# Kernel optimization log

Hardware: AMD Instinct MI355X
Metric: run time of the kernel (lower is better)

Reference implementation:

```python
import jax, jax.numpy as jnp
import numpy as np

B, L, D = 128, 256, 1024


def setup_inputs() -> dict:
    key = jax.random.key(0)
    k = jax.random.split(key, 6)
    return {
        "tok0": jax.random.normal(k[0], (B, L, D), jnp.float32),
        "tok1": jax.random.normal(k[1], (B, L, D), jnp.float32),
        "glob0": jax.random.normal(k[2], (B, D), jnp.float32),
        "glob1": jax.random.normal(k[3], (B, D), jnp.float32),
        "len0": jax.random.randint(k[4], (B,), 0, L),
        "len1": jax.random.randint(k[5], (B,), 0, L),
    }


def _side_sums(tok, glob, lens):
    """JSD expectations for one view.

    Equivalent to the original ragged concat + dense mask construction:
    non-positive entries of get_positive_expectation contribute
    -softplus(0) + log2 = 0, and positive entries of
    get_negative_expectation contribute softplus(0) + 0 - log2 = 0,
    so only the masked terms below survive. Padding tokens (l >= lens[b])
    never exist in the original concatenated matrix, so they are excluded.
    """
    b, l_max = tok.shape[0], tok.shape[1]
    # scores: token x sentence-global, [B, L, B]
    res = jnp.einsum("bld,gd->blg", tok, glob)
    valid = jnp.arange(l_max)[None, :] < lens[:, None]          # [B, L]
    same = jnp.eye(b, dtype=bool)[:, None, :]                    # [B, 1, B]
    pos = valid[:, :, None] & same                               # token vs own sentence
    neg = valid[:, :, None] & ~same                              # token vs other sentences
    e_pos = jnp.sum(jnp.where(pos, -jax.nn.softplus(-res), 0.0))
    e_neg = jnp.sum(jnp.where(neg, jax.nn.softplus(-res) + res, 0.0))
    return e_pos, e_neg


def reference(tok0, tok1, glob0, glob1, len0, len1):
    len0 = jnp.clip(len0, 1, None)
    len1 = jnp.clip(len1, 1, None)
    avg_sentence_length = (jnp.mean(len0.astype(jnp.float32))
                           + jnp.mean(len1.astype(jnp.float32))) / 2.0

    ep0, en0 = _side_sums(tok0, glob0, len0)
    ep1, en1 = _side_sums(tok1, glob1, len1)

    num_nodes = (jnp.sum(len0) + jnp.sum(len1)).astype(jnp.float32)
    num_graphs = jnp.float32(B)
    e_pos = (ep0 + ep1) / num_nodes
    e_neg = (en0 + en1) / (num_nodes * (num_graphs - 1.0))
    loss = e_neg - e_pos
    return loss, avg_sentence_length
```

## Files before the change

kernel.cpp:

```cpp
#include <hip/hip_runtime.h>
#include <hip/hip_bf16.h>

#define B_SENT 128
#define L_TOK  256
#define D_DIM  1024
#define TM     64
#define BK     32
#define NKB    (D_DIM / BK)

typedef __attribute__((ext_vector_type(8))) short bf16x8;
typedef __attribute__((ext_vector_type(4))) float f32x4;

__device__ __forceinline__ unsigned short f2bf(float f) {
    return __builtin_bit_cast(unsigned short, __float2bfloat16(f));
}
__device__ __forceinline__ float softplus_f(float x) {
    float ax = fabsf(x);
    return fmaxf(x, 0.0f) + __logf(1.0f + __expf(-ax));
}
__device__ __forceinline__ bf16x8 cvt8f(const float4& lo, const float4& hi) {
    bf16x8 u;
    u[0] = (short)f2bf(lo.x); u[1] = (short)f2bf(lo.y);
    u[2] = (short)f2bf(lo.z); u[3] = (short)f2bf(lo.w);
    u[4] = (short)f2bf(hi.x); u[5] = (short)f2bf(hi.y);
    u[6] = (short)f2bf(hi.z); u[7] = (short)f2bf(hi.w);
    return u;
}

__device__ __forceinline__ void gl_lds16(const void* g, void* l) {
    __builtin_amdgcn_global_load_lds(
        (const __attribute__((address_space(1))) unsigned int*)g,
        (__attribute__((address_space(3))) unsigned int*)l, 16, 0, 0);
}

__global__ __launch_bounds__(256) void pack_g_kernel(
    const float* __restrict__ g0, const float* __restrict__ g1,
    short* __restrict__ packed)
{
    const int idx  = blockIdx.x * 256 + threadIdx.x;
    const int lane = idx & 63;
    const int n    = (idx >> 6) & 7;
    const int kb   = (idx >> 9) & 31;
    const int side = idx >> 14;
    const int row  = n * 16 + (lane & 15);
    const int col  = kb * 32 + (lane >> 4) * 8;
    const float* g = side ? g1 : g0;
    const float4 v0 = *reinterpret_cast<const float4*>(&g[(size_t)row * D_DIM + col]);
    const float4 v1 = *reinterpret_cast<const float4*>(&g[(size_t)row * D_DIM + col + 4]);
    *reinterpret_cast<bf16x8*>(&packed[(size_t)idx * 8]) = cvt8f(v0, v1);
}

__global__ __launch_bounds__(256, 4) void mi_main_kernel(
    const float* __restrict__ tok0, const float* __restrict__ tok1,
    const int* __restrict__ len0, const int* __restrict__ len1,
    const short* __restrict__ packed, float* __restrict__ acc_ws)
{
    const int side = blockIdx.y;
    const float* tok = side ? tok1 : tok0;
    const int*   len = side ? len1 : len0;

    const int tile   = blockIdx.x;
    const int tb     = tile * TM;
    const int b_sent = tile >> 2;
    const int count  = max(1, len[b_sent]) - (tile & 3) * TM;
    if (count <= 0) return;

    const int tid  = threadIdx.x;
    const int wave = tid >> 6;
    const int lane = tid & 63;
    const int lrow = lane & 15;
    const int kgrp = lane >> 4;

    __shared__ float As[2][2048];
    __shared__ short Bs[2][4096];
    __shared__ float sred[8];

    const float* asrc = tok + (size_t)(tb + wave * 16 + lrow) * D_DIM + kgrp * 8;
    const short* bchunk = packed + (size_t)side * NKB * 4096;
    const int br0 = ((wave * 2 + 0) * 64 + lane) * 8;
    const int br1 = ((wave * 2 + 1) * 64 + lane) * 8;

    f32x4 acc[8];
#pragma unroll
    for (int n = 0; n < 8; ++n) acc[n] = (f32x4){0.f, 0.f, 0.f, 0.f};

    auto stage = [&](int buf, int kb) {
        const float* a = asrc + kb * BK;
        gl_lds16(a,     &As[buf][(wave * 2 + 0) * 256]);
        gl_lds16(a + 4, &As[buf][(wave * 2 + 1) * 256]);
        const short* bc = bchunk + (size_t)kb * 4096;
        gl_lds16(bc + br0, &Bs[buf][(wave * 2 + 0) * 512]);
        gl_lds16(bc + br1, &Bs[buf][(wave * 2 + 1) * 512]);
    };

    auto compute = [&](int buf) {
        const f32x4 alo = *reinterpret_cast<const f32x4*>(
            &As[buf][(wave * 2 + 0) * 256 + lane * 4]);
        const f32x4 ahi = *reinterpret_cast<const f32x4*>(
            &As[buf][(wave * 2 + 1) * 256 + lane * 4]);
        bf16x8 af;
        af[0] = (short)f2bf(alo[0]); af[1] = (short)f2bf(alo[1]);
        af[2] = (short)f2bf(alo[2]); af[3] = (short)f2bf(alo[3]);
        af[4] = (short)f2bf(ahi[0]); af[5] = (short)f2bf(ahi[1]);
        af[6] = (short)f2bf(ahi[2]); af[7] = (short)f2bf(ahi[3]);
#pragma unroll
        for (int n = 0; n < 8; ++n) {
            bf16x8 b = *reinterpret_cast<const bf16x8*>(&Bs[buf][(n * 64 + lane) * 8]);
            acc[n] = __builtin_amdgcn_mfma_f32_16x16x32_bf16(af, b, acc[n], 0, 0, 0);
        }
    };

    stage(0, 0);
    __syncthreads();
#pragma unroll 1
    for (int kb = 0; kb < NKB; ++kb) {
        const int cur = kb & 1;
        if (kb + 1 < NKB) stage(cur ^ 1, kb + 1);
        compute(cur);
        __syncthreads();
    }

    float ep = 0.f, en = 0.f;
#pragma unroll
    for (int n = 0; n < 8; ++n) {
        const int g = n * 16 + lrow;
#pragma unroll
        for (int j = 0; j < 4; ++j) {
            const int rl = wave * 16 + kgrp * 4 + j;
            if (rl < count) {
                float res = acc[n][j];
                float sp  = softplus_f(res);
                if (g == b_sent) ep += res - sp;
                else             en += sp;
            }
        }
    }

#pragma unroll
    for (int off = 32; off; off >>= 1) {
        ep += __shfl_down(ep, off);
        en += __shfl_down(en, off);
    }
    if (lane == 0) { sred[wave * 2] = ep; sred[wave * 2 + 1] = en; }
    __syncthreads();
    if (tid == 0) {
        float tep = sred[0] + sred[2] + sred[4] + sred[6];
        float ten = sred[1] + sred[3] + sred[5] + sred[7];
        atomicAdd(&acc_ws[side * 2 + 0], tep);
        atomicAdd(&acc_ws[side * 2 + 1], ten);
    }
}

__global__ void mi_finalize_kernel(const int* __restrict__ len0,
                                   const int* __restrict__ len1,
                                   const float* __restrict__ acc_ws,
                                   float* __restrict__ out)
{
    const int lane = threadIdx.x;
    int s0 = 0, s1 = 0;
    for (int i = lane; i < B_SENT; i += 64) {
        s0 += max(1, len0[i]);
        s1 += max(1, len1[i]);
    }
#pragma unroll
    for (int off = 32; off; off >>= 1) {
        s0 += __shfl_down(s0, off);
        s1 += __shfl_down(s1, off);
    }
    if (lane == 0) {
        const float num_nodes = (float)(s0 + s1);
        const float ep = acc_ws[0] + acc_ws[2];
        const float en = acc_ws[1] + acc_ws[3];
        out[0] = en / (num_nodes * (float)(B_SENT - 1)) - ep / num_nodes;
        out[1] = ((float)s0 + (float)s1) / (2.0f * (float)B_SENT);
    }
}

extern "C" void kernel_launch(void* const* d_in, const int* in_sizes, int n_in,
                              void* d_out, int out_size, void* d_ws, size_t ws_size,
                              hipStream_t stream) {
    const float* tok0  = (const float*)d_in[0];
    const float* tok1  = (const float*)d_in[1];
    const float* glob0 = (const float*)d_in[2];
    const float* glob1 = (const float*)d_in[3];
    const int*   len0  = (const int*)d_in[4];
    const int*   len1  = (const int*)d_in[5];
    float* out = (float*)d_out;

    float* acc    = (float*)d_ws;
    short* packed = (short*)((char*)d_ws + 256);

    hipMemsetAsync(d_ws, 0, 256, stream);
    pack_g_kernel<<<128, 256, 0, stream>>>(glob0, glob1, packed);

    dim3 grid(32768 / TM, 2);
    mi_main_kernel<<<grid, 256, 0, stream>>>(tok0, tok1, len0, len1, packed, acc);
    mi_finalize_kernel<<<1, 64, 0, stream>>>(len0, len1, acc, out);
}
```

Baseline: 62.76 us.

## Use 128-row tiles with 512 threads and triple-buffered LDS pipeline

Doubles the token tile to 128 rows per block with 8 waves, so each packed glob chunk loaded into LDS is shared by twice as many rows. The double buffer with full __syncthreads becomes a three-stage ring using explicit vmcnt waits and a raw barrier, which lets two stages of loads stay in flight while computing. Rows past the sentence length are clamped to the last valid row so no out-of-range memory is read. Larger blocks coarsen the skipping of padded tiles, so more wasted MFMA work is done on ragged lengths, and the larger LDS footprint may reduce occupancy.

```diff
diff --git a/kernel.cpp b/kernel.cpp
--- a/kernel.cpp
+++ b/kernel.cpp
@@ -4,12 +4,14 @@
 #define B_SENT 128
 #define L_TOK  256
 #define D_DIM  1024
-#define TM     64
+#define TM     128
 #define BK     32
 #define NKB    (D_DIM / BK)
 
 typedef __attribute__((ext_vector_type(8))) short bf16x8;
 typedef __attribute__((ext_vector_type(4))) float f32x4;
+
+#define WAITVM(N) asm volatile("s_waitcnt vmcnt(" #N ")" ::: "memory")
 
 __device__ __forceinline__ unsigned short f2bf(float f) {
     return __builtin_bit_cast(unsigned short, __float2bfloat16(f));
@@ -50,7 +52,7 @@
     *reinterpret_cast<bf16x8*>(&packed[(size_t)idx * 8]) = cvt8f(v0, v1);
 }
 
-__global__ __launch_bounds__(256, 4) void mi_main_kernel(
+__global__ __launch_bounds__(512, 4) void mi_main_kernel(
     const float* __restrict__ tok0, const float* __restrict__ tok1,
     const int* __restrict__ len0, const int* __restrict__ len1,
     const short* __restrict__ packed, float* __restrict__ acc_ws)
@@ -60,9 +62,10 @@
     const int*   len = side ? len1 : len0;
 
     const int tile   = blockIdx.x;
-    const int tb     = tile * TM;
-    const int b_sent = tile >> 2;
-    const int count  = max(1, len[b_sent]) - (tile & 3) * TM;
+    const int b_sent = tile >> 1;
+    const int half   = tile & 1;
+    const int tb     = b_sent * L_TOK + half * TM;
+    const int count  = max(1, len[b_sent]) - half * TM;
     if (count <= 0) return;
 
     const int tid  = threadIdx.x;
@@ -71,14 +74,14 @@
     const int lrow = lane & 15;
     const int kgrp = lane >> 4;
 
-    __shared__ float As[2][2048];
-    __shared__ short Bs[2][4096];
-    __shared__ float sred[8];
-
-    const float* asrc = tok + (size_t)(tb + wave * 16 + lrow) * D_DIM + kgrp * 8;
+    __shared__ float As[3][4096];
+    __shared__ short Bs[3][4096];
+    __shared__ float sred[16];
+
+    const int arow = min(wave * 16 + lrow, count - 1);
+    const float* asrc = tok + (size_t)(tb + arow) * D_DIM + kgrp * 8;
     const short* bchunk = packed + (size_t)side * NKB * 4096;
-    const int br0 = ((wave * 2 + 0) * 64 + lane) * 8;
-    const int br1 = ((wave * 2 + 1) * 64 + lane) * 8;
+    const int boff = (wave * 64 + lane) * 8;
 
     f32x4 acc[8];
 #pragma unroll
@@ -88,9 +91,7 @@
         const float* a = asrc + kb * BK;
         gl_lds16(a,     &As[buf][(wave * 2 + 0) * 256]);
         gl_lds16(a + 4, &As[buf][(wave * 2 + 1) * 256]);
-        const short* bc = bchunk + (size_t)kb * 4096;
-        gl_lds16(bc + br0, &Bs[buf][(wave * 2 + 0) * 512]);
-        gl_lds16(bc + br1, &Bs[buf][(wave * 2 + 1) * 512]);
+        gl_lds16(bchunk + (size_t)kb * 4096 + boff, &Bs[buf][wave * 512]);
     };
 
     auto compute = [&](int buf) {
@@ -111,14 +112,19 @@
     };
 
     stage(0, 0);
-    __syncthreads();
+    stage(1, 1);
 #pragma unroll 1
-    for (int kb = 0; kb < NKB; ++kb) {
-        const int cur = kb & 1;
-        if (kb + 1 < NKB) stage(cur ^ 1, kb + 1);
-        compute(cur);
-        __syncthreads();
-    }
+    for (int kb = 0; kb < NKB - 1; ++kb) {
+        WAITVM(3);
+        __builtin_amdgcn_s_barrier();
+        asm volatile("" ::: "memory");
+        if (kb + 2 < NKB) stage((kb + 2) % 3, kb + 2);
+        compute(kb % 3);
+    }
+    WAITVM(0);
+    __builtin_amdgcn_s_barrier();
+    asm volatile("" ::: "memory");
+    compute((NKB - 1) % 3);
 
     float ep = 0.f, en = 0.f;
 #pragma unroll
@@ -144,8 +150,9 @@
     if (lane == 0) { sred[wave * 2] = ep; sred[wave * 2 + 1] = en; }
     __syncthreads();
     if (tid == 0) {
-        float tep = sred[0] + sred[2] + sred[4] + sred[6];
-        float ten = sred[1] + sred[3] + sred[5] + sred[7];
+        float tep = 0.f, ten = 0.f;
+#pragma unroll
+        for (int w = 0; w < 8; ++w) { tep += sred[w * 2]; ten += sred[w * 2 + 1]; }
         atomicAdd(&acc_ws[side * 2 + 0], tep);
         atomicAdd(&acc_ws[side * 2 + 1], ten);
     }
@@ -194,6 +201,6 @@
     pack_g_kernel<<<128, 256, 0, stream>>>(glob0, glob1, packed);
 
     dim3 grid(32768 / TM, 2);
-    mi_main_kernel<<<grid, 256, 0, stream>>>(tok0, tok1, len0, len1, packed, acc);
+    mi_main_kernel<<<grid, 512, 0, stream>>>(tok0, tok1, len0, len1, packed, acc);
     mi_finalize_kernel<<<1, 64, 0, stream>>>(len0, len1, acc, out);
 }
```

New measurement: 56.28 us. 10.3% less time.

## Split N across two blocks, deepen LDS pipeline to four stages, clamp padded rows

Applied to the files above, without the earlier changes.

Each token tile is now handled by two blocks, each covering half of the 128 sentence columns. This doubles the grid and halves per-block MFMA work and accumulators, but each A tile is loaded twice. The K loop moves from a double buffer with __syncthreads to a 4-deep buffer that keeps three global-to-LDS loads in flight, using explicit vmcnt waits and barriers. Rows past the sentence length are clamped to a valid row, which avoids reading tokens that will be masked anyway.

```diff
diff --git a/kernel.cpp b/kernel.cpp
--- a/kernel.cpp
+++ b/kernel.cpp
@@ -5,8 +5,10 @@
 #define L_TOK  256
 #define D_DIM  1024
 #define TM     64
+#define TN     64
 #define BK     32
 #define NKB    (D_DIM / BK)
+#define NBUF   4
 
 typedef __attribute__((ext_vector_type(8))) short bf16x8;
 typedef __attribute__((ext_vector_type(4))) float f32x4;
@@ -18,12 +20,12 @@
     float ax = fabsf(x);
     return fmaxf(x, 0.0f) + __logf(1.0f + __expf(-ax));
 }
-__device__ __forceinline__ bf16x8 cvt8f(const float4& lo, const float4& hi) {
+__device__ __forceinline__ bf16x8 cvt8f(const f32x4& lo, const f32x4& hi) {
     bf16x8 u;
-    u[0] = (short)f2bf(lo.x); u[1] = (short)f2bf(lo.y);
-    u[2] = (short)f2bf(lo.z); u[3] = (short)f2bf(lo.w);
-    u[4] = (short)f2bf(hi.x); u[5] = (short)f2bf(hi.y);
-    u[6] = (short)f2bf(hi.z); u[7] = (short)f2bf(hi.w);
+    u[0] = (short)f2bf(lo[0]); u[1] = (short)f2bf(lo[1]);
+    u[2] = (short)f2bf(lo[2]); u[3] = (short)f2bf(lo[3]);
+    u[4] = (short)f2bf(hi[0]); u[5] = (short)f2bf(hi[1]);
+    u[6] = (short)f2bf(hi[2]); u[7] = (short)f2bf(hi[3]);
     return u;
 }
 
@@ -45,8 +47,8 @@
     const int row  = n * 16 + (lane & 15);
     const int col  = kb * 32 + (lane >> 4) * 8;
     const float* g = side ? g1 : g0;
-    const float4 v0 = *reinterpret_cast<const float4*>(&g[(size_t)row * D_DIM + col]);
-    const float4 v1 = *reinterpret_cast<const float4*>(&g[(size_t)row * D_DIM + col + 4]);
+    const f32x4 v0 = *reinterpret_cast<const f32x4*>(&g[(size_t)row * D_DIM + col]);
+    const f32x4 v1 = *reinterpret_cast<const f32x4*>(&g[(size_t)row * D_DIM + col + 4]);
     *reinterpret_cast<bf16x8*>(&packed[(size_t)idx * 8]) = cvt8f(v0, v1);
 }
 
@@ -59,9 +61,11 @@
     const float* tok = side ? tok1 : tok0;
     const int*   len = side ? len1 : len0;
 
-    const int tile   = blockIdx.x;
-    const int tb     = tile * TM;
+    const int bx     = blockIdx.x;
+    const int tile   = bx >> 1;
+    const int nh     = bx & 1;
     const int b_sent = tile >> 2;
+    const int tb     = b_sent * L_TOK + (tile & 3) * TM;
     const int count  = max(1, len[b_sent]) - (tile & 3) * TM;
     if (count <= 0) return;
 
@@ -71,26 +75,24 @@
     const int lrow = lane & 15;
     const int kgrp = lane >> 4;
 
-    __shared__ float As[2][2048];
-    __shared__ short Bs[2][4096];
+    __shared__ float As[NBUF][2048];
+    __shared__ short Bs[NBUF][2048];
     __shared__ float sred[8];
 
-    const float* asrc = tok + (size_t)(tb + wave * 16 + lrow) * D_DIM + kgrp * 8;
+    const int arow = min(wave * 16 + lrow, count - 1);
+    const float* asrc = tok + (size_t)(tb + arow) * D_DIM + kgrp * 8;
     const short* bchunk = packed + (size_t)side * NKB * 4096;
-    const int br0 = ((wave * 2 + 0) * 64 + lane) * 8;
-    const int br1 = ((wave * 2 + 1) * 64 + lane) * 8;
-
-    f32x4 acc[8];
-#pragma unroll
-    for (int n = 0; n < 8; ++n) acc[n] = (f32x4){0.f, 0.f, 0.f, 0.f};
+    const int boff = ((nh * 4 + wave) * 64 + lane) * 8;
+
+    f32x4 acc[4];
+#pragma unroll
+    for (int n = 0; n < 4; ++n) acc[n] = (f32x4){0.f, 0.f, 0.f, 0.f};
 
     auto stage = [&](int buf, int kb) {
         const float* a = asrc + kb * BK;
         gl_lds16(a,     &As[buf][(wave * 2 + 0) * 256]);
         gl_lds16(a + 4, &As[buf][(wave * 2 + 1) * 256]);
-        const short* bc = bchunk + (size_t)kb * 4096;
-        gl_lds16(bc + br0, &Bs[buf][(wave * 2 + 0) * 512]);
-        gl_lds16(bc + br1, &Bs[buf][(wave * 2 + 1) * 512]);
+        gl_lds16(bchunk + (size_t)kb * 4096 + boff, &Bs[buf][wave * 512]);
     };
 
     auto compute = [&](int buf) {
@@ -98,32 +100,38 @@
             &As[buf][(wave * 2 + 0) * 256 + lane * 4]);
         const f32x4 ahi = *reinterpret_cast<const f32x4*>(
             &As[buf][(wave * 2 + 1) * 256 + lane * 4]);
-        bf16x8 af;
-        af[0] = (short)f2bf(alo[0]); af[1] = (short)f2bf(alo[1]);
-        af[2] = (short)f2bf(alo[2]); af[3] = (short)f2bf(alo[3]);
-        af[4] = (short)f2bf(ahi[0]); af[5] = (short)f2bf(ahi[1]);
-        af[6] = (short)f2bf(ahi[2]); af[7] = (short)f2bf(ahi[3]);
-#pragma unroll
-        for (int n = 0; n < 8; ++n) {
+        const bf16x8 af = cvt8f(alo, ahi);
+#pragma unroll
+        for (int n = 0; n < 4; ++n) {
             bf16x8 b = *reinterpret_cast<const bf16x8*>(&Bs[buf][(n * 64 + lane) * 8]);
             acc[n] = __builtin_amdgcn_mfma_f32_16x16x32_bf16(af, b, acc[n], 0, 0, 0);
         }
     };
 
+#define WAITSTEP(N) do {                                                     \
+        asm volatile("s_waitcnt vmcnt(" #N ")" ::: "memory");                \
+        __builtin_amdgcn_s_barrier();                                        \
+        __builtin_amdgcn_sched_barrier(0);                                   \
+    } while (0)
+
     stage(0, 0);
-    __syncthreads();
+    stage(1, 1);
+    stage(2, 2);
 #pragma unroll 1
-    for (int kb = 0; kb < NKB; ++kb) {
-        const int cur = kb & 1;
-        if (kb + 1 < NKB) stage(cur ^ 1, kb + 1);
-        compute(cur);
-        __syncthreads();
-    }
+    for (int kb = 0; kb < NKB - 3; ++kb) {
+        WAITSTEP(6);
+        stage((kb + 3) & 3, kb + 3);
+        compute(kb & 3);
+    }
+    WAITSTEP(6); compute((NKB - 3) & 3);
+    WAITSTEP(3); compute((NKB - 2) & 3);
+    WAITSTEP(0); compute((NKB - 1) & 3);
+#undef WAITSTEP
 
     float ep = 0.f, en = 0.f;
 #pragma unroll
-    for (int n = 0; n < 8; ++n) {
-        const int g = n * 16 + lrow;
+    for (int n = 0; n < 4; ++n) {
+        const int g = nh * TN + n * 16 + lrow;
 #pragma unroll
         for (int j = 0; j < 4; ++j) {
             const int rl = wave * 16 + kgrp * 4 + j;
@@ -193,7 +201,7 @@
     hipMemsetAsync(d_ws, 0, 256, stream);
     pack_g_kernel<<<128, 256, 0, stream>>>(glob0, glob1, packed);
 
-    dim3 grid(32768 / TM, 2);
+    dim3 grid(1024, 2);
     mi_main_kernel<<<grid, 256, 0, stream>>>(tok0, tok1, len0, len1, packed, acc);
     mi_finalize_kernel<<<1, 64, 0, stream>>>(len0, len1, acc, out);
 }
```

Result: slower. 102.8 us (+63.8%).

## Split K across eight waves with 16-row tiles and an LDS tree reduction

Applied to the files above, without the earlier changes.

The main kernel now works on 16-token tiles with 512 threads. Each of the eight waves handles a 128-wide slice of the D dimension, loading its A and B fragments straight from global memory into registers instead of staging them through double-buffered LDS. The partial accumulators are then combined with a three-level LDS tree reduction before the softplus epilogue. Finer tiles skip more padding rows and the K-split exposes more parallelism, but each block re-reads all of packed B, which raises L2 traffic, and the kernel holds many live registers.

```diff
diff --git a/kernel.cpp b/kernel.cpp
--- a/kernel.cpp
+++ b/kernel.cpp
@@ -4,9 +4,7 @@
 #define B_SENT 128
 #define L_TOK  256
 #define D_DIM  1024
-#define TM     64
-#define BK     32
-#define NKB    (D_DIM / BK)
+#define TM     16
 
 typedef __attribute__((ext_vector_type(8))) short bf16x8;
 typedef __attribute__((ext_vector_type(4))) float f32x4;
@@ -18,19 +16,13 @@
     float ax = fabsf(x);
     return fmaxf(x, 0.0f) + __logf(1.0f + __expf(-ax));
 }
-__device__ __forceinline__ bf16x8 cvt8f(const float4& lo, const float4& hi) {
+__device__ __forceinline__ bf16x8 cvt8f(const f32x4& lo, const f32x4& hi) {
     bf16x8 u;
-    u[0] = (short)f2bf(lo.x); u[1] = (short)f2bf(lo.y);
-    u[2] = (short)f2bf(lo.z); u[3] = (short)f2bf(lo.w);
-    u[4] = (short)f2bf(hi.x); u[5] = (short)f2bf(hi.y);
-    u[6] = (short)f2bf(hi.z); u[7] = (short)f2bf(hi.w);
+    u[0] = (short)f2bf(lo[0]); u[1] = (short)f2bf(lo[1]);
+    u[2] = (short)f2bf(lo[2]); u[3] = (short)f2bf(lo[3]);
+    u[4] = (short)f2bf(hi[0]); u[5] = (short)f2bf(hi[1]);
+    u[6] = (short)f2bf(hi[2]); u[7] = (short)f2bf(hi[3]);
     return u;
-}
-
-__device__ __forceinline__ void gl_lds16(const void* g, void* l) {
-    __builtin_amdgcn_global_load_lds(
-        (const __attribute__((address_space(1))) unsigned int*)g,
-        (__attribute__((address_space(3))) unsigned int*)l, 16, 0, 0);
 }
 
 __global__ __launch_bounds__(256) void pack_g_kernel(
@@ -45,12 +37,12 @@
     const int row  = n * 16 + (lane & 15);
     const int col  = kb * 32 + (lane >> 4) * 8;
     const float* g = side ? g1 : g0;
-    const float4 v0 = *reinterpret_cast<const float4*>(&g[(size_t)row * D_DIM + col]);
-    const float4 v1 = *reinterpret_cast<const float4*>(&g[(size_t)row * D_DIM + col + 4]);
+    const f32x4 v0 = *reinterpret_cast<const f32x4*>(&g[(size_t)row * D_DIM + col]);
+    const f32x4 v1 = *reinterpret_cast<const f32x4*>(&g[(size_t)row * D_DIM + col + 4]);
     *reinterpret_cast<bf16x8*>(&packed[(size_t)idx * 8]) = cvt8f(v0, v1);
 }
 
-__global__ __launch_bounds__(256, 4) void mi_main_kernel(
+__global__ __launch_bounds__(512, 2) void mi_main_kernel(
     const float* __restrict__ tok0, const float* __restrict__ tok1,
     const int* __restrict__ len0, const int* __restrict__ len1,
     const short* __restrict__ packed, float* __restrict__ acc_ws)
@@ -60,10 +52,11 @@
     const int*   len = side ? len1 : len0;
 
     const int tile   = blockIdx.x;
-    const int tb     = tile * TM;
-    const int b_sent = tile >> 2;
-    const int count  = max(1, len[b_sent]) - (tile & 3) * TM;
+    const int b_sent = tile >> 4;
+    const int toff   = (tile & 15) * TM;
+    const int count  = max(1, len[b_sent]) - toff;
     if (count <= 0) return;
+    const int tb     = b_sent * L_TOK + toff;
 
     const int tid  = threadIdx.x;
     const int wave = tid >> 6;
@@ -71,83 +64,94 @@
     const int lrow = lane & 15;
     const int kgrp = lane >> 4;
 
-    __shared__ float As[2][2048];
-    __shared__ short Bs[2][4096];
-    __shared__ float sred[8];
-
-    const float* asrc = tok + (size_t)(tb + wave * 16 + lrow) * D_DIM + kgrp * 8;
-    const short* bchunk = packed + (size_t)side * NKB * 4096;
-    const int br0 = ((wave * 2 + 0) * 64 + lane) * 8;
-    const int br1 = ((wave * 2 + 1) * 64 + lane) * 8;
+    const short* bchunk = packed + ((size_t)side * 32 + wave * 4) * 4096;
+    bf16x8 Bk[4][8];
+#pragma unroll
+    for (int s = 0; s < 4; ++s)
+#pragma unroll
+        for (int n = 0; n < 8; ++n)
+            Bk[s][n] = *reinterpret_cast<const bf16x8*>(
+                bchunk + (size_t)s * 4096 + (n * 64 + lane) * 8);
+
+    const int arow = min(lrow, count - 1);
+    const float* asrc = tok + (size_t)(tb + arow) * D_DIM + wave * 128 + kgrp * 8;
+    f32x4 Alo[4], Ahi[4];
+#pragma unroll
+    for (int s = 0; s < 4; ++s) {
+        Alo[s] = *reinterpret_cast<const f32x4*>(asrc + s * 32);
+        Ahi[s] = *reinterpret_cast<const f32x4*>(asrc + s * 32 + 4);
+    }
 
     f32x4 acc[8];
 #pragma unroll
     for (int n = 0; n < 8; ++n) acc[n] = (f32x4){0.f, 0.f, 0.f, 0.f};
-
-    auto stage = [&](int buf, int kb) {
-        const float* a = asrc + kb * BK;
-        gl_lds16(a,     &As[buf][(wave * 2 + 0) * 256]);
-        gl_lds16(a + 4, &As[buf][(wave * 2 + 1) * 256]);
-        const short* bc = bchunk + (size_t)kb * 4096;
-        gl_lds16(bc + br0, &Bs[buf][(wave * 2 + 0) * 512]);
-        gl_lds16(bc + br1, &Bs[buf][(wave * 2 + 1) * 512]);
-    };
-
-    auto compute = [&](int buf) {
-        const f32x4 alo = *reinterpret_cast<const f32x4*>(
-            &As[buf][(wave * 2 + 0) * 256 + lane * 4]);
-        const f32x4 ahi = *reinterpret_cast<const f32x4*>(
-            &As[buf][(wave * 2 + 1) * 256 + lane * 4]);
-        bf16x8 af;
-        af[0] = (short)f2bf(alo[0]); af[1] = (short)f2bf(alo[1]);
-        af[2] = (short)f2bf(alo[2]); af[3] = (short)f2bf(alo[3]);
-        af[4] = (short)f2bf(ahi[0]); af[5] = (short)f2bf(ahi[1]);
-        af[6] = (short)f2bf(ahi[2]); af[7] = (short)f2bf(ahi[3]);
+#pragma unroll
+    for (int s = 0; s < 4; ++s) {
+        const bf16x8 af = cvt8f(Alo[s], Ahi[s]);
+#pragma unroll
+        for (int n = 0; n < 8; ++n)
+            acc[n] = __builtin_amdgcn_mfma_f32_16x16x32_bf16(af, Bk[s][n], acc[n], 0, 0, 0);
+    }
+
+    __shared__ f32x4 cl[4][64][9];
+    if (wave >= 4) {
+#pragma unroll
+        for (int n = 0; n < 8; ++n) cl[wave - 4][lane][n] = acc[n];
+    }
+    __syncthreads();
+    if (wave < 4) {
 #pragma unroll
         for (int n = 0; n < 8; ++n) {
-            bf16x8 b = *reinterpret_cast<const bf16x8*>(&Bs[buf][(n * 64 + lane) * 8]);
-            acc[n] = __builtin_amdgcn_mfma_f32_16x16x32_bf16(af, b, acc[n], 0, 0, 0);
-        }
-    };
-
-    stage(0, 0);
-    __syncthreads();
-#pragma unroll 1
-    for (int kb = 0; kb < NKB; ++kb) {
-        const int cur = kb & 1;
-        if (kb + 1 < NKB) stage(cur ^ 1, kb + 1);
-        compute(cur);
-        __syncthreads();
-    }
-
-    float ep = 0.f, en = 0.f;
-#pragma unroll
-    for (int n = 0; n < 8; ++n) {
-        const int g = n * 16 + lrow;
-#pragma unroll
-        for (int j = 0; j < 4; ++j) {
-            const int rl = wave * 16 + kgrp * 4 + j;
-            if (rl < count) {
-                float res = acc[n][j];
-                float sp  = softplus_f(res);
-                if (g == b_sent) ep += res - sp;
-                else             en += sp;
+            f32x4 o = cl[wave][lane][n];
+            acc[n][0] += o[0]; acc[n][1] += o[1]; acc[n][2] += o[2]; acc[n][3] += o[3];
+        }
+    }
+    __syncthreads();
+    if (wave == 2 || wave == 3) {
+#pragma unroll
+        for (int n = 0; n < 8; ++n) cl[wave - 2][lane][n] = acc[n];
+    }
+    __syncthreads();
+    if (wave < 2) {
+#pragma unroll
+        for (int n = 0; n < 8; ++n) {
+            f32x4 o = cl[wave][lane][n];
+            acc[n][0] += o[0]; acc[n][1] += o[1]; acc[n][2] += o[2]; acc[n][3] += o[3];
+        }
+    }
+    __syncthreads();
+    if (wave == 1) {
+#pragma unroll
+        for (int n = 0; n < 8; ++n) cl[0][lane][n] = acc[n];
+    }
+    __syncthreads();
+
+    if (wave == 0) {
+        float ep = 0.f, en = 0.f;
+#pragma unroll
+        for (int n = 0; n < 8; ++n) {
+            f32x4 o = cl[0][lane][n];
+            const int g = n * 16 + lrow;
+#pragma unroll
+            for (int j = 0; j < 4; ++j) {
+                const int rl = kgrp * 4 + j;
+                if (rl < count) {
+                    float res = acc[n][j] + o[j];
+                    float sp  = softplus_f(res);
+                    if (g == b_sent) ep += res - sp;
+                    else             en += sp;
+                }
             }
         }
-    }
-
-#pragma unroll
-    for (int off = 32; off; off >>= 1) {
-        ep += __shfl_down(ep, off);
-        en += __shfl_down(en, off);
-    }
-    if (lane == 0) { sred[wave * 2] = ep; sred[wave * 2 + 1] = en; }
-    __syncthreads();
-    if (tid == 0) {
-        float tep = sred[0] + sred[2] + sred[4] + sred[6];
-        float ten = sred[1] + sred[3] + sred[5] + sred[7];
-        atomicAdd(&acc_ws[side * 2 + 0], tep);
-        atomicAdd(&acc_ws[side * 2 + 1], ten);
+#pragma unroll
+        for (int off = 32; off; off >>= 1) {
+            ep += __shfl_down(ep, off);
+            en += __shfl_down(en, off);
+        }
+        if (lane == 0) {
+            atomicAdd(&acc_ws[side * 2 + 0], ep);
+            atomicAdd(&acc_ws[side * 2 + 1], en);
+        }
     }
 }
 
@@ -194,6 +198,6 @@
     pack_g_kernel<<<128, 256, 0, stream>>>(glob0, glob1, packed);
 
     dim3 grid(32768 / TM, 2);
-    mi_main_kernel<<<grid, 256, 0, stream>>>(tok0, tok1, len0, len1, packed, acc);
+    mi_main_kernel<<<grid, 512, 0, stream>>>(tok0, tok1, len0, len1, packed, acc);
     mi_finalize_kernel<<<1, 64, 0, stream>>>(len0, len1, acc, out);
 }
```

Result: slower. 99.26 us (+58.2%).
